# Kernel tuning notes

Hardware: AMD Instinct MI355X
Metric: run time of the kernel (lower is better)

The kernel has to match this reference:

```python
import jax, jax.numpy as jnp
import numpy as np

STRIDES = (2, 2, 2)  # from init_kwargs


def _sparse_conv3d_transpose(images, kernel, default_value, base_plane, strides):
    """Sparse masked 3D transposed conv driven by a per-pixel depth base plane.

    images:     [B, Hi, Wi, Di, C]  stored slab of active voxels per pixel
    kernel:     [kH, kW, kD, F, C]
    base_plane: [B, Ho, Wo, 1] int  starting VIRTUAL depth of the output slab
    Output virtual depth of voxel (ho, wo, do) is base_plane[ho, wo] + do.
    Input slab start (in input-depth units) at input pixel (hi, wi) is
    base_plane[hi*sH, wi*sW] // sD. SAME-style padding ((k-1)//2).
    Out-of-slab / out-of-bounds taps read default_value (frozen zero).
    """
    B, Hi, Wi, Di, C = images.shape
    k0, k1, k2, F, _ = kernel.shape
    s0, s1, s2 = strides
    bp = base_plane[..., 0]                       # [B, Ho, Wo]
    Ho, Wo = bp.shape[1], bp.shape[2]
    Do = Di * s2
    p0, p1, p2 = (k0 - 1) // 2, (k1 - 1) // 2, (k2 - 1) // 2
    bp_in = bp[:, ::s0, ::s1] // s2               # [B, Hi, Wi] input slab start
    b_idx = jnp.arange(B)[:, None, None]
    vd = bp[..., None] + jnp.arange(Do)           # [B, Ho, Wo, Do] virtual out depth
    ho = jnp.arange(Ho)
    wo = jnp.arange(Wo)
    out = jnp.zeros((B, Ho, Wo, Do, F), images.dtype)
    for kh in range(k0):
        hn = ho + p0 - kh
        hok = (hn % s0 == 0) & (hn >= 0) & (hn < Hi * s0)
        hi = jnp.clip(hn // s0, 0, Hi - 1)
        for kw in range(k1):
            wn = wo + p1 - kw
            wok = (wn % s1 == 0) & (wn >= 0) & (wn < Wi * s1)
            wi = jnp.clip(wn // s1, 0, Wi - 1)
            sp_ok = hok[None, :, None] & wok[None, None, :]              # [1,Ho,Wo]
            bpg = bp_in[b_idx, hi[None, :, None], wi[None, None, :]]     # [B,Ho,Wo]
            for kd in range(k2):
                dn = vd + p2 - kd                                        # [B,Ho,Wo,Do]
                dok = (dn % s2) == 0
                di = dn // s2 - bpg[..., None]
                mask = sp_ok[..., None] & dok & (di >= 0) & (di < Di)
                dic = jnp.clip(di, 0, Di - 1)
                # gather [B,Ho,Wo,Do,C]
                vals = images[b_idx[..., None], hi[None, :, None, None],
                              wi[None, None, :, None], dic]
                vals = jnp.where(mask[..., None], vals, default_value)
                out = out + jnp.einsum('bhwdc,fc->bhwdf', vals, kernel[kh, kw, kd])
    return out


def setup_inputs() -> dict:
    key = jax.random.key(0)
    k1, k2, k3 = jax.random.split(key, 3)
    B, Hi, Wi, Di, C, F = 2, 64, 64, 32, 16, 8
    images = jax.random.normal(k1, (B, Hi, Wi, Di, C), dtype=jnp.float32)
    base_plane = jax.random.randint(k2, (B, Hi * 2, Wi * 2, 1), 0, 16, dtype=jnp.int32)
    kernel = jax.random.normal(k3, (3, 3, 3, F, C), dtype=jnp.float32) * 0.1
    default_value = jnp.zeros((), dtype=jnp.float32)  # frozen, zeros initializer
    return {"images": images, "base_plane": base_plane,
            "kernel": kernel, "default_value": default_value}


def reference(images, base_plane, kernel, default_value):
    return _sparse_conv3d_transpose(images, kernel, default_value, base_plane, STRIDES)
```

## Files before the change

### kernel.cpp

```cpp
#include <hip/hip_runtime.h>

constexpr int Bc  = 2;
constexpr int HiC = 64, WiC = 64, DiC = 32;
constexpr int Cc  = 16, Fc  = 8;
constexpr int HoC = 128, WoC = 128, DoC = 64;

constexpr int SLAB_SHORTS = DiC * Cc;
constexpr int NSLAB       = 10;
constexpr int ZOFF        = NSLAB * SLAB_SHORTS * 2;

typedef __attribute__((ext_vector_type(8))) short short8;
typedef __attribute__((ext_vector_type(4))) float f32x4;

__device__ alignas(16) const float FZERO[8] = {0, 0, 0, 0, 0, 0, 0, 0};

__device__ __forceinline__ unsigned pk2(float x, float y) {
    unsigned ux = __float_as_uint(x), uy = __float_as_uint(y);
    ux += ((ux >> 16) & 1u) + 0x7FFFu;
    uy += ((uy >> 16) & 1u) + 0x7FFFu;
    return (ux >> 16) | (uy & 0xFFFF0000u);
}
__device__ __forceinline__ short8 pack8(float4 a, float4 b) {
    union { unsigned u[4]; short8 s; } r;
    r.u[0] = pk2(a.x, a.y); r.u[1] = pk2(a.z, a.w);
    r.u[2] = pk2(b.x, b.y); r.u[3] = pk2(b.z, b.w);
    return r.s;
}

template<int CLS>
__device__ __forceinline__ void doCols(const short* __restrict__ slabs,
                                       const int*   __restrict__ bp,
                                       const float* __restrict__ kern,
                                       float*       __restrict__ out,
                                       float*       __restrict__ ldsw,
                                       int b, int ho, int wo0, int wi0, int lane) {
    constexpr int NP = (CLS == 0) ? 1 : ((CLS == 3) ? 4 : 2);
    constexpr int OP = (NP + 1) / 2;
    constexpr int KH[4][4] = {{1,0,0,0},{1,1,0,0},{0,2,0,0},{0,0,2,2}};
    constexpr int KW[4][4] = {{1,0,0,0},{0,2,0,0},{1,1,0,0},{0,2,0,2}};

    const int quad = lane >> 4, n = lane & 15;
    const int half = quad >> 1, chalf = quad & 1;
    const int chalfB = chalf * 16;

    short8 bE[NP], bO[OP];
    #pragma unroll
    for (int p = 0; p < NP; ++p) {
        const int kp = KH[CLS][p] * 3 + KW[CLS][p];
        const float* wp = (n < Fc)
            ? kern + (kp * 3 + 2 * half) * 128 + n * 16 + chalf * 8 : FZERO;
        bE[p] = pack8(*(const float4*)wp, *(const float4*)(wp + 4));
    }
    #pragma unroll
    for (int pp = 0; pp < OP; ++pp) {
        const int  PA   = (2 * pp < NP) ? 2 * pp : 0;
        const bool hasB = (2 * pp + 1) < NP;
        const int  PB   = hasB ? (2 * pp + 1) : 0;
        const int kpa = KH[CLS][PA] * 3 + KW[CLS][PA];
        const int kpb = KH[CLS][PB] * 3 + KW[CLS][PB];
        const int kp  = half ? kpb : kpa;
        const bool v  = (n < Fc) && (!half || hasB);
        const float* wp = v ? kern + (kp * 3 + 1) * 128 + n * 16 + chalf * 8 : FZERO;
        bO[pp] = pack8(*(const float4*)wp, *(const float4*)(wp + 4));
    }

    int colx[4], bpcol[4], bpgr[4][NP], pxo[4][NP]; bool pvs[4][NP];
    #pragma unroll
    for (int cc = 0; cc < 4; ++cc) {
        const int wo = wo0 + 2 * cc;
        colx[cc]  = __builtin_amdgcn_readfirstlane((b * HoC + ho) * WoC + wo);
        bpcol[cc] = bp[colx[cc]];
        #pragma unroll
        for (int p = 0; p < NP; ++p) {
            const int kh = KH[CLS][p], kw = KW[CLS][p];
            int hi = (ho + 1 - kh) >> 1; hi = hi > HiC - 1 ? HiC - 1 : hi;
            int wi = (wo + 1 - kw) >> 1; wi = wi > WiC - 1 ? WiC - 1 : wi;
            pvs[cc][p] = (kh != 0 || ho + 1 < HoC) && (kw != 0 || wo + 1 < WoC);
            const int sidx =
                __builtin_amdgcn_readfirstlane((b * HoC + 2 * hi) * WoC + 2 * wi);
            bpgr[cc][p] = bp[sidx];
            const int hidx = (kh == 0) ? 1 : 0;
            pxo[cc][p] = __builtin_amdgcn_readfirstlane(
                             (hidx * 5 + (wi - wi0)) << 10);
        }
    }

    #pragma unroll
    for (int cc = 0; cc < 4; ++cc) {
        const int bp_col = bpcol[cc];
        const int q      = (bp_col + 1) & 1;
        const int baseE  = (bp_col + q + 1) >> 1;
        const int baseO  = (bp_col + 1 - q) >> 1;
        int sE[NP], sO[NP];
        #pragma unroll
        for (int p = 0; p < NP; ++p) {
            const int bpg = bpgr[cc][p] >> 1;
            sE[p] = pvs[cc][p] ? baseE - bpg : -100000;
            sO[p] = pvs[cc][p] ? baseO - bpg : -100000;
        }

        short8 aE[2][NP], aO[2][OP];
        #pragma unroll
        for (int g = 0; g < 2; ++g) {
            #pragma unroll
            for (int p = 0; p < NP; ++p) {
                const int  di = sE[p] + 16 * g + n - half;
                const bool ok = (unsigned)di < (unsigned)DiC;
                const int  off = ok ? pxo[cc][p] + di * 32 + chalfB : ZOFF;
                aE[g][p] = *(const short8*)((const char*)slabs + off);
            }
            #pragma unroll
            for (int pp = 0; pp < OP; ++pp) {
                const int  PA   = (2 * pp < NP) ? 2 * pp : 0;
                const bool hasB = (2 * pp + 1) < NP;
                const int  PB   = hasB ? (2 * pp + 1) : 0;
                const int  sOs  = half ? (hasB ? sO[PB] : -100000) : sO[PA];
                const int  pxs  = half ? pxo[cc][PB] : pxo[cc][PA];
                const int  di = sOs + 16 * g + n;
                const bool ok = (unsigned)di < (unsigned)DiC;
                const int  off = ok ? pxs + di * 32 + chalfB : ZOFF;
                aO[g][pp] = *(const short8*)((const char*)slabs + off);
            }
        }

        f32x4 accE[2] = {{0.f,0.f,0.f,0.f},{0.f,0.f,0.f,0.f}};
        f32x4 accO[2] = {{0.f,0.f,0.f,0.f},{0.f,0.f,0.f,0.f}};
        #pragma unroll
        for (int g = 0; g < 2; ++g) {
            #pragma unroll
            for (int p = 0; p < NP; ++p)
                accE[g] = __builtin_amdgcn_mfma_f32_16x16x32_bf16(aE[g][p], bE[p], accE[g], 0, 0, 0);
            #pragma unroll
            for (int pp = 0; pp < OP; ++pp)
                accO[g] = __builtin_amdgcn_mfma_f32_16x16x32_bf16(aO[g][pp], bO[pp], accO[g], 0, 0, 0);
        }

        __builtin_amdgcn_wave_barrier();
        if (n < Fc) {
            #pragma unroll
            for (int g = 0; g < 2; ++g) {
                #pragma unroll
                for (int r = 0; r < 4; ++r) {
                    const int m2 = 16 * g + quad * 4 + r;
                    ldsw[(2 * m2 + q) * Fc + n]     = accE[g][r];
                    ldsw[(2 * m2 + 1 - q) * Fc + n] = accO[g][r];
                }
            }
        }
        __builtin_amdgcn_wave_barrier();
        float* outc = out + (size_t)colx[cc] * (DoC * Fc);
        *(float4*)(outc + lane * 8)     = *(const float4*)(ldsw + lane * 8);
        *(float4*)(outc + lane * 8 + 4) = *(const float4*)(ldsw + lane * 8 + 4);
        __builtin_amdgcn_wave_barrier();
    }
}

__global__ __launch_bounds__(256, 4)
void sconv_mfma(const float* __restrict__ img, const int* __restrict__ bp,
                const float* __restrict__ kern, float* __restrict__ out) {
    __shared__ short slabs[NSLAB * SLAB_SHORTS + 8];
    __shared__ float lds[4 * DoC * Fc];
    const int t = threadIdx.x, wv = t >> 6, lane = t & 63;
    const int b = blockIdx.z, r = blockIdx.y;
    const int p  = wv & 1, hs = wv >> 1;
    const int wo0 = (blockIdx.x << 3) + p;
    const int wi0 = blockIdx.x << 2;
    const int ho  = 2 * r + hs;
    float* ldsw = lds + wv * (DoC * Fc);

    const int hi0 = r;
    int hi1 = r + 1; if (hi1 > HiC - 1) hi1 = HiC - 1;
    #pragma unroll
    for (int k = 0; k < 3; ++k) {
        const int s = wv + 4 * k;
        if (s < NSLAB) {
            const int hi = (s >= 5) ? hi1 : hi0;
            int wi = wi0 + ((s >= 5) ? s - 5 : s); if (wi > WiC - 1) wi = WiC - 1;
            const float* g = img + (((b * HiC + hi) * WiC + wi) << 9) + lane * 8;
            float4 v0 = *(const float4*)g;
            float4 v1 = *(const float4*)(g + 4);
            *(short8*)&slabs[(s << 9) + lane * 8] = pack8(v0, v1);
        }
    }
    if (t < 8) slabs[NSLAB * SLAB_SHORTS + t] = 0;
    __syncthreads();

    if (hs) {
        if (p) doCols<3>(slabs, bp, kern, out, ldsw, b, ho, wo0, wi0, lane);
        else   doCols<2>(slabs, bp, kern, out, ldsw, b, ho, wo0, wi0, lane);
    } else {
        if (p) doCols<1>(slabs, bp, kern, out, ldsw, b, ho, wo0, wi0, lane);
        else   doCols<0>(slabs, bp, kern, out, ldsw, b, ho, wo0, wi0, lane);
    }
}

extern "C" void kernel_launch(void* const* d_in, const int* in_sizes, int n_in,
                              void* d_out, int out_size, void* d_ws, size_t ws_size,
                              hipStream_t stream) {
    const float* images = (const float*)d_in[0];
    const int*   bp     = (const int*)d_in[1];
    const float* kern   = (const float*)d_in[2];
    float* out = (float*)d_out;
    (void)d_ws; (void)ws_size;

    dim3 grid(WoC / 8, HoC / 2, Bc), block(256);
    hipLaunchKernelGGL(sconv_mfma, grid, block, 0, stream,
                       images, bp, kern, out);
}
```

Before: 95.24 us.

## Process four row-pairs per block with double-buffered slabs and hoisted weights

Each block now loops over four consecutive input rows instead of one, which cuts the grid by a factor of four. The bf16-packed kernel weights are built once per wave and reused across the loop rather than reloaded per row. Slab staging alternates between two LDS buffers with one __syncthreads per iteration, and occupancy bounds drop from 4 to 2 blocks per CU. The loop reloads both input rows on every iteration rather than reusing the shared row, and fewer blocks may reduce parallelism and latency hiding.

```diff
diff --git a/kernel.cpp b/kernel.cpp
--- a/kernel.cpp
+++ b/kernel.cpp
@@ -7,6 +7,7 @@
 
 constexpr int SLAB_SHORTS = DiC * Cc;
 constexpr int NSLAB       = 10;
+constexpr int BUF_SHORTS  = NSLAB * SLAB_SHORTS + 8;
 constexpr int ZOFF        = NSLAB * SLAB_SHORTS * 2;
 
 typedef __attribute__((ext_vector_type(8))) short short8;
@@ -27,42 +28,53 @@
     return r.s;
 }
 
+constexpr int KHT[4][4] = {{1,0,0,0},{1,1,0,0},{0,2,0,0},{0,0,2,2}};
+constexpr int KWT[4][4] = {{1,0,0,0},{0,2,0,0},{1,1,0,0},{0,2,0,2}};
+
+
+template<int CLS>
+__device__ __forceinline__ void buildB(const float* __restrict__ kern, int lane,
+                                       short8* __restrict__ bE,
+                                       short8* __restrict__ bO) {
+    constexpr int NP = (CLS == 0) ? 1 : ((CLS == 3) ? 4 : 2);
+    constexpr int OP = (NP + 1) / 2;
+    const int quad = lane >> 4, n = lane & 15;
+    const int half = quad >> 1, chalf = quad & 1;
+    #pragma unroll
+    for (int p = 0; p < NP; ++p) {
+        const int kp = KHT[CLS][p] * 3 + KWT[CLS][p];
+        const float* wp = (n < Fc)
+            ? kern + (kp * 3 + 2 * half) * 128 + n * 16 + chalf * 8 : FZERO;
+        bE[p] = pack8(*(const float4*)wp, *(const float4*)(wp + 4));
+    }
+    #pragma unroll
+    for (int pp = 0; pp < OP; ++pp) {
+        const int  PA   = (2 * pp < NP) ? 2 * pp : 0;
+        const bool hasB = (2 * pp + 1) < NP;
+        const int  PB   = hasB ? (2 * pp + 1) : 0;
+        const int kpa = KHT[CLS][PA] * 3 + KWT[CLS][PA];
+        const int kpb = KHT[CLS][PB] * 3 + KWT[CLS][PB];
+        const int kp  = half ? kpb : kpa;
+        const bool v  = (n < Fc) && (!half || hasB);
+        const float* wp = v ? kern + (kp * 3 + 1) * 128 + n * 16 + chalf * 8 : FZERO;
+        bO[pp] = pack8(*(const float4*)wp, *(const float4*)(wp + 4));
+    }
+}
+
 template<int CLS>
 __device__ __forceinline__ void doCols(const short* __restrict__ slabs,
                                        const int*   __restrict__ bp,
-                                       const float* __restrict__ kern,
+                                       const short8* __restrict__ bE,
+                                       const short8* __restrict__ bO,
                                        float*       __restrict__ out,
                                        float*       __restrict__ ldsw,
                                        int b, int ho, int wo0, int wi0, int lane) {
     constexpr int NP = (CLS == 0) ? 1 : ((CLS == 3) ? 4 : 2);
     constexpr int OP = (NP + 1) / 2;
-    constexpr int KH[4][4] = {{1,0,0,0},{1,1,0,0},{0,2,0,0},{0,0,2,2}};
-    constexpr int KW[4][4] = {{1,0,0,0},{0,2,0,0},{1,1,0,0},{0,2,0,2}};
 
     const int quad = lane >> 4, n = lane & 15;
     const int half = quad >> 1, chalf = quad & 1;
     const int chalfB = chalf * 16;
-
-    short8 bE[NP], bO[OP];
-    #pragma unroll
-    for (int p = 0; p < NP; ++p) {
-        const int kp = KH[CLS][p] * 3 + KW[CLS][p];
-        const float* wp = (n < Fc)
-            ? kern + (kp * 3 + 2 * half) * 128 + n * 16 + chalf * 8 : FZERO;
-        bE[p] = pack8(*(const float4*)wp, *(const float4*)(wp + 4));
-    }
-    #pragma unroll
-    for (int pp = 0; pp < OP; ++pp) {
-        const int  PA   = (2 * pp < NP) ? 2 * pp : 0;
-        const bool hasB = (2 * pp + 1) < NP;
-        const int  PB   = hasB ? (2 * pp + 1) : 0;
-        const int kpa = KH[CLS][PA] * 3 + KW[CLS][PA];
-        const int kpb = KH[CLS][PB] * 3 + KW[CLS][PB];
-        const int kp  = half ? kpb : kpa;
-        const bool v  = (n < Fc) && (!half || hasB);
-        const float* wp = v ? kern + (kp * 3 + 1) * 128 + n * 16 + chalf * 8 : FZERO;
-        bO[pp] = pack8(*(const float4*)wp, *(const float4*)(wp + 4));
-    }
 
     int colx[4], bpcol[4], bpgr[4][NP], pxo[4][NP]; bool pvs[4][NP];
     #pragma unroll
@@ -72,7 +84,7 @@
         bpcol[cc] = bp[colx[cc]];
         #pragma unroll
         for (int p = 0; p < NP; ++p) {
-            const int kh = KH[CLS][p], kw = KW[CLS][p];
+            const int kh = KHT[CLS][p], kw = KWT[CLS][p];
             int hi = (ho + 1 - kh) >> 1; hi = hi > HiC - 1 ? HiC - 1 : hi;
             int wi = (wo + 1 - kw) >> 1; wi = wi > WiC - 1 ? WiC - 1 : wi;
             pvs[cc][p] = (kh != 0 || ho + 1 < HoC) && (kw != 0 || wo + 1 < WoC);
@@ -155,42 +167,55 @@
     }
 }
 
-__global__ __launch_bounds__(256, 4)
+__global__ __launch_bounds__(256, 2)
 void sconv_mfma(const float* __restrict__ img, const int* __restrict__ bp,
                 const float* __restrict__ kern, float* __restrict__ out) {
-    __shared__ short slabs[NSLAB * SLAB_SHORTS + 8];
+    __shared__ short slabs2[2][BUF_SHORTS];
     __shared__ float lds[4 * DoC * Fc];
     const int t = threadIdx.x, wv = t >> 6, lane = t & 63;
-    const int b = blockIdx.z, r = blockIdx.y;
+    const int b = blockIdx.z, rg = blockIdx.y;
     const int p  = wv & 1, hs = wv >> 1;
     const int wo0 = (blockIdx.x << 3) + p;
     const int wi0 = blockIdx.x << 2;
-    const int ho  = 2 * r + hs;
     float* ldsw = lds + wv * (DoC * Fc);
 
-    const int hi0 = r;
-    int hi1 = r + 1; if (hi1 > HiC - 1) hi1 = HiC - 1;
-    #pragma unroll
-    for (int k = 0; k < 3; ++k) {
-        const int s = wv + 4 * k;
-        if (s < NSLAB) {
-            const int hi = (s >= 5) ? hi1 : hi0;
-            int wi = wi0 + ((s >= 5) ? s - 5 : s); if (wi > WiC - 1) wi = WiC - 1;
-            const float* g = img + (((b * HiC + hi) * WiC + wi) << 9) + lane * 8;
-            float4 v0 = *(const float4*)g;
-            float4 v1 = *(const float4*)(g + 4);
-            *(short8*)&slabs[(s << 9) + lane * 8] = pack8(v0, v1);
-        }
-    }
-    if (t < 8) slabs[NSLAB * SLAB_SHORTS + t] = 0;
-    __syncthreads();
-
-    if (hs) {
-        if (p) doCols<3>(slabs, bp, kern, out, ldsw, b, ho, wo0, wi0, lane);
-        else   doCols<2>(slabs, bp, kern, out, ldsw, b, ho, wo0, wi0, lane);
-    } else {
-        if (p) doCols<1>(slabs, bp, kern, out, ldsw, b, ho, wo0, wi0, lane);
-        else   doCols<0>(slabs, bp, kern, out, ldsw, b, ho, wo0, wi0, lane);
+    short8 bE[4], bO[2];
+    if (hs) { if (p) buildB<3>(kern, lane, bE, bO); else buildB<2>(kern, lane, bE, bO); }
+    else    { if (p) buildB<1>(kern, lane, bE, bO); else buildB<0>(kern, lane, bE, bO); }
+
+    if (t < 8) {
+        slabs2[0][NSLAB * SLAB_SHORTS + t] = 0;
+        slabs2[1][NSLAB * SLAB_SHORTS + t] = 0;
+    }
+
+    for (int rr = 0; rr < 4; ++rr) {
+        const int r  = (rg << 2) + rr;
+        const int ho = 2 * r + hs;
+        short* sb = &slabs2[rr & 1][0];
+
+        const int hi0 = r;
+        int hi1 = r + 1; if (hi1 > HiC - 1) hi1 = HiC - 1;
+        #pragma unroll
+        for (int k = 0; k < 3; ++k) {
+            const int s = wv + 4 * k;
+            if (s < NSLAB) {
+                const int hi = (s >= 5) ? hi1 : hi0;
+                int wi = wi0 + ((s >= 5) ? s - 5 : s); if (wi > WiC - 1) wi = WiC - 1;
+                const float* g = img + (((b * HiC + hi) * WiC + wi) << 9) + lane * 8;
+                float4 v0 = *(const float4*)g;
+                float4 v1 = *(const float4*)(g + 4);
+                *(short8*)&sb[(s << 9) + lane * 8] = pack8(v0, v1);
+            }
+        }
+        __syncthreads();
+
+        if (hs) {
+            if (p) doCols<3>(sb, bp, bE, bO, out, ldsw, b, ho, wo0, wi0, lane);
+            else   doCols<2>(sb, bp, bE, bO, out, ldsw, b, ho, wo0, wi0, lane);
+        } else {
+            if (p) doCols<1>(sb, bp, bE, bO, out, ldsw, b, ho, wo0, wi0, lane);
+            else   doCols<0>(sb, bp, bE, bO, out, ldsw, b, ho, wo0, wi0, lane);
+        }
     }
 }
 
@@ -203,7 +228,7 @@
     float* out = (float*)d_out;
     (void)d_ws; (void)ws_size;
 
-    dim3 grid(WoC / 8, HoC / 2, Bc), block(256);
+    dim3 grid(WoC / 8, 16, Bc), block(256);
     hipLaunchKernelGGL(sconv_mfma, grid, block, 0, stream,
                        images, bp, kern, out);
 }
```

New measurement: 99.52 us. 4.5% more time.
